# Kernel optimization log

Hardware: AMD Instinct MI355X
Metric: run time of the kernel (lower is better)

The kernel has to match this reference:

```python
import jax, jax.numpy as jnp
import numpy as np

SEQ, WORD, EMBED, NHEAD = 2048, 1024, 128, 16


def setup_inputs() -> dict:
    key = jax.random.key(0)
    ks = jax.random.split(key, 6)
    sw = 1.0 / np.sqrt(WORD)  # xavier-ish scale for linear weights
    sp = 1.0 / np.sqrt(EMBED * NHEAD)
    return {
        "x": jax.random.normal(ks[0], (SEQ, WORD), jnp.float32),
        "Wq": jax.random.normal(ks[1], (NHEAD, WORD, EMBED), jnp.float32) * sw,
        "bq": jnp.zeros((NHEAD, EMBED), jnp.float32),
        "Wk": jax.random.normal(ks[2], (NHEAD, WORD, EMBED), jnp.float32) * sw,
        "bk": jnp.zeros((NHEAD, EMBED), jnp.float32),
        "Wv": jax.random.normal(ks[3], (NHEAD, WORD, EMBED), jnp.float32) * sw,
        "bv": jnp.zeros((NHEAD, EMBED), jnp.float32),
        "proj": jax.random.normal(ks[4], (NHEAD * EMBED, EMBED), jnp.float32) * sp,
    }


def reference(x, Wq, bq, Wk, bk, Wv, bv, proj):
    # Batched-head equivalent of the per-head Attention ModuleList loop.
    # x: [S, W]; Wq/Wk/Wv: [H, W, E]; b*: [H, E]; proj: [H*E, E]
    Q = jnp.einsum("sw,hwe->hse", x, Wq) + bq[:, None, :]
    K = jnp.einsum("sw,hwe->hse", x, Wk) + bk[:, None, :]
    V = jnp.einsum("sw,hwe->hse", x, Wv) + bv[:, None, :]
    scale = 1.0 / jnp.sqrt(jnp.asarray(EMBED, x.dtype))
    scores = jnp.einsum("hqe,hke->hqk", Q, K) * scale  # [H, S, S]
    attn = jax.nn.softmax(scores, axis=-1)
    Z = jnp.einsum("hqk,hke->hqe", attn, V)  # [H, S, E]
    # torch.cat([...], dim=1): per-head outputs side-by-side -> [S, H*E]
    Z_s = jnp.transpose(Z, (1, 0, 2)).reshape(x.shape[0], -1)
    return Z_s @ proj  # [S, E]
```

## Files before the change

kernel.cpp:

```cpp
#include <hip/hip_runtime.h>
#include <stdint.h>

#define GAS __attribute__((address_space(1)))
#define LAS __attribute__((address_space(3)))

typedef unsigned short u16;
typedef __attribute__((ext_vector_type(8))) __bf16 bf16x8;
typedef __attribute__((ext_vector_type(4))) float f32x4;

#define SEQ 2048
#define WORD 1024
#define EMBED 128
#define NHEAD 16

__device__ __forceinline__ u16 f2b(float f) {
  return __builtin_bit_cast(u16, (__bf16)f);
}

__global__ __launch_bounds__(256) void cast_x_kernel(const float* __restrict__ x,
                                                     u16* __restrict__ xb) {
  int i = (blockIdx.x * 256 + threadIdx.x) * 4;
  float4 v = *(const float4*)(x + i);
  ushort4 o;
  o.x = f2b(v.x); o.y = f2b(v.y); o.z = f2b(v.z); o.w = f2b(v.w);
  *(ushort4*)(xb + i) = o;
}

__global__ __launch_bounds__(256) void transpose_cast_kernel(
    const float* __restrict__ s0, const float* __restrict__ s1,
    const float* __restrict__ s2, u16* __restrict__ d0, u16* __restrict__ d1,
    u16* __restrict__ d2, int R, int C, long stride, int zsel) {
  __shared__ float tile[32][33];
  const float* s;
  u16* d;
  if (zsel) {
    int z = blockIdx.z;
    int wsel = z >> 4, hh = z & 15;
    s = (wsel == 0 ? s0 : wsel == 1 ? s1 : s2) + (long)hh * stride;
    d = (wsel == 0 ? d0 : wsel == 1 ? d1 : d2) + (long)hh * stride;
  } else {
    s = s0; d = d0;
  }
  int r0 = blockIdx.x * 32, c0 = blockIdx.y * 32;
  int tx = threadIdx.x & 31, ty = threadIdx.x >> 5;
#pragma unroll
  for (int i = 0; i < 4; ++i)
    tile[ty + i * 8][tx] = s[(long)(r0 + ty + i * 8) * C + c0 + tx];
  __syncthreads();
#pragma unroll
  for (int i = 0; i < 4; ++i)
    d[(long)(c0 + ty + i * 8) * R + r0 + tx] = f2b(tile[tx][ty + i * 8]);
}

template <typename OUT>
__device__ __forceinline__ void gemm128(const u16* __restrict__ A, const u16* __restrict__ B,
                                        OUT* __restrict__ C, int lda, int ldb, int ldc,
                                        int ksteps, const float* biasN, const float* biasM,
                                        float scale) {
  __shared__ u16 lA[128 * 64];
  __shared__ u16 lB[128 * 64];
  const int tid = threadIdx.x;
  const int l = tid & 63, w = tid >> 6;
  const int quad = l >> 4, ln = l & 15;
  const int wm = w >> 1, wn = w & 1;
  f32x4 acc[4][4] = {};
  for (int ks = 0; ks < ksteps; ++ks) {
    const u16* Ak = A + ks * 64;
    const u16* Bk = B + ks * 64;
    __syncthreads();
#pragma unroll
    for (int i = 0; i < 4; ++i) {
      int idx = w * 256 + i * 64 + l;
      int r = idx >> 3, cp = idx & 7;
      int cg = cp ^ (r & 7);
      __builtin_amdgcn_global_load_lds((const GAS void*)(Ak + (long)r * lda + cg * 8),
                                       (LAS void*)(lA + (w * 256 + i * 64) * 8), 16, 0, 0);
      __builtin_amdgcn_global_load_lds((const GAS void*)(Bk + (long)r * ldb + cg * 8),
                                       (LAS void*)(lB + (w * 256 + i * 64) * 8), 16, 0, 0);
    }
    __syncthreads();
    bf16x8 af[2][4], bfv[2][4];
#pragma unroll
    for (int kc = 0; kc < 2; ++kc) {
#pragma unroll
      for (int i = 0; i < 4; ++i) {
        int c = kc * 4 + quad;
        int rm = wm * 64 + i * 16 + ln;
        af[kc][i] = *(const bf16x8*)(lA + rm * 64 + ((c ^ (rm & 7)) * 8));
        int rn = wn * 64 + i * 16 + ln;
        bfv[kc][i] = *(const bf16x8*)(lB + rn * 64 + ((c ^ (rn & 7)) * 8));
      }
    }
#pragma unroll
    for (int kc = 0; kc < 2; ++kc)
#pragma unroll
      for (int i = 0; i < 4; ++i)
#pragma unroll
        for (int j = 0; j < 4; ++j)
          acc[i][j] = __builtin_amdgcn_mfma_f32_16x16x32_bf16(af[kc][i], bfv[kc][j],
                                                              acc[i][j], 0, 0, 0);
  }
#pragma unroll
  for (int i = 0; i < 4; ++i) {
#pragma unroll
    for (int j = 0; j < 4; ++j) {
      int row0 = wm * 64 + i * 16 + quad * 4;
      int col = wn * 64 + j * 16 + ln;
      float bn = biasN ? biasN[col] : 0.f;
#pragma unroll
      for (int reg = 0; reg < 4; ++reg) {
        int row = row0 + reg;
        float bm = biasM ? biasM[row] : 0.f;
        float v = (acc[i][j][reg] + bn + bm) * scale;
        if constexpr (sizeof(OUT) == 2)
          C[(long)row * ldc + col] = (OUT)f2b(v);
        else
          C[(long)row * ldc + col] = v;
      }
    }
  }
}

__global__ __launch_bounds__(256, 3) void qkv_gemm_kernel(
    const u16* __restrict__ xb, const u16* __restrict__ Wqt, const u16* __restrict__ Wkt,
    const u16* __restrict__ Wvt, const float* __restrict__ bq, const float* __restrict__ bk,
    const float* __restrict__ bv, u16* __restrict__ Q, u16* __restrict__ Kb,
    u16* __restrict__ Vt) {
  const int t = blockIdx.x;
  const int h = blockIdx.y;
  const int which = blockIdx.z;
  const float qscale = 0.12753042123789493f;
  if (which == 0) {
    gemm128<u16>(xb + t * 128 * WORD, Wqt + h * EMBED * WORD,
                 Q + h * SEQ * EMBED + t * 128 * EMBED, WORD, WORD, EMBED,
                 WORD / 64, bq + h * EMBED, nullptr, qscale);
  } else if (which == 1) {
    gemm128<u16>(xb + t * 128 * WORD, Wkt + h * EMBED * WORD,
                 Kb + h * SEQ * EMBED + t * 128 * EMBED, WORD, WORD, EMBED,
                 WORD / 64, bk + h * EMBED, nullptr, 1.f);
  } else {
    gemm128<u16>(Wvt + h * EMBED * WORD, xb + t * 128 * WORD,
                 Vt + h * EMBED * SEQ + t * 128, WORD, WORD, SEQ,
                 WORD / 64, nullptr, bv + h * EMBED, 1.f);
  }
}

__global__ __launch_bounds__(256, 1) void attn_kernel(const u16* __restrict__ Q,
                                                      const u16* __restrict__ K,
                                                      const u16* __restrict__ V,
                                                      u16* __restrict__ Zs) {
  __shared__ u16 lKV[2][2][16384];
  __shared__ u16 lP[4 * 16 * 72];
  const int h = blockIdx.y, qb = blockIdx.x;
  const int tid = threadIdx.x;
  const int l = tid & 63, w = tid >> 6, quad = l >> 4, ln = l & 15;
  const int wr = w >> 1, wk = w & 1;
  const u16* Qh = Q + h * SEQ * EMBED;
  const u16* Kh = K + h * SEQ * EMBED;
  const u16* Vh = V + h * EMBED * SEQ;
  u16* Pw = lP + w * (16 * 72);
  const int q0 = qb * 128 + wr * 64;

  bf16x8 qf[4][4];
#pragma unroll
  for (int rs = 0; rs < 4; ++rs)
#pragma unroll
    for (int kc = 0; kc < 4; ++kc)
      qf[rs][kc] = *(const bf16x8*)(Qh + (q0 + rs * 16 + ln) * EMBED + kc * 32 + quad * 8);

  const __bf16 ov = (ln == 0) ? (__bf16)1.0f : (__bf16)0.0f;
  const bf16x8 onesf = {ov, ov, ov, ov, ov, ov, ov, ov};

  f32x4 oacc[4][8] = {};
  f32x4 lacc[4] = {};

  auto stage = [&](int sup, int buf) {
#pragma unroll
    for (int j = 0; j < 8; ++j) {
      int cb = j * 256 + w * 64;
      int c = cb + l;
      int r = c >> 4, sc = c & 15, cg = sc ^ (r & 15);
      __builtin_amdgcn_global_load_lds(
          (const GAS void*)(Kh + (sup * 128 + r) * EMBED + cg * 8),
          (LAS void*)(&lKV[buf][0][cb * 8]), 16, 0, 0);
      __builtin_amdgcn_global_load_lds(
          (const GAS void*)(Vh + r * SEQ + sup * 128 + cg * 8),
          (LAS void*)(&lKV[buf][1][cb * 8]), 16, 0, 0);
    }
  };

  stage(0, 0);
  for (int sup = 0; sup < SEQ / 128; ++sup) {
    const int cur = sup & 1;
    __syncthreads();
    if (sup + 1 < SEQ / 128) stage(sup + 1, cur ^ 1);
    const u16* Kb = lKV[cur][0];
    const u16* Vb = lKV[cur][1];
    f32x4 sacc[4][4] = {};
#pragma unroll
    for (int kc = 0; kc < 4; ++kc) {
      bf16x8 kf[4];
#pragma unroll
      for (int ns = 0; ns < 4; ++ns) {
        int kr = wk * 64 + ns * 16 + ln;
        kf[ns] = *(const bf16x8*)(Kb + kr * 128 + (((kc * 4 + quad) ^ (kr & 15)) * 8));
      }
#pragma unroll
      for (int ns = 0; ns < 4; ++ns)
#pragma unroll
        for (int rs = 0; rs < 4; ++rs)
          sacc[rs][ns] = __builtin_amdgcn_mfma_f32_16x16x32_bf16(qf[rs][kc], kf[ns],
                                                                 sacc[rs][ns], 0, 0, 0);
    }
    bf16x8 vf[2][8];
#pragma unroll
    for (int kc2 = 0; kc2 < 2; ++kc2)
#pragma unroll
      for (int es = 0; es < 8; ++es) {
        int er = es * 16 + ln;
        vf[kc2][es] = *(const bf16x8*)(
            Vb + er * 128 + (((wk * 8 + kc2 * 4 + quad) ^ (er & 15)) * 8));
      }
#pragma unroll
    for (int rs = 0; rs < 4; ++rs) {
#pragma unroll
      for (int ns = 0; ns < 4; ++ns)
#pragma unroll
        for (int r = 0; r < 4; ++r)
          Pw[(quad * 4 + r) * 72 + ns * 16 + ln] = f2b(exp2f(sacc[rs][ns][r]));
#pragma unroll
      for (int kc2 = 0; kc2 < 2; ++kc2) {
        bf16x8 pa = *(const bf16x8*)(Pw + ln * 72 + kc2 * 32 + quad * 8);
#pragma unroll
        for (int es = 0; es < 8; ++es)
          oacc[rs][es] = __builtin_amdgcn_mfma_f32_16x16x32_bf16(pa, vf[kc2][es],
                                                                 oacc[rs][es], 0, 0, 0);
        lacc[rs] = __builtin_amdgcn_mfma_f32_16x16x32_bf16(pa, onesf, lacc[rs], 0, 0, 0);
      }
    }
  }
  __syncthreads();
  float* lO = (float*)lKV;
  if (wk == 1) {
#pragma unroll
    for (int rs = 0; rs < 4; ++rs) {
#pragma unroll
      for (int es = 0; es < 8; ++es)
#pragma unroll
        for (int r = 0; r < 4; ++r)
          lO[(wr * 64 + rs * 16 + quad * 4 + r) * 132 + es * 16 + ln] = oacc[rs][es][r];
      if (ln == 0)
#pragma unroll
        for (int r = 0; r < 4; ++r)
          lO[(wr * 64 + rs * 16 + quad * 4 + r) * 132 + 128] = lacc[rs][r];
    }
  }
  __syncthreads();
  if (wk == 0) {
#pragma unroll
    for (int rs = 0; rs < 4; ++rs)
#pragma unroll
      for (int r = 0; r < 4; ++r) {
        int grow = wr * 64 + rs * 16 + quad * 4 + r;
        float lsum = __shfl(lacc[rs][r], l & 48) + lO[grow * 132 + 128];
        float rl = 1.f / lsum;
        int srow = qb * 128 + grow;
#pragma unroll
        for (int es = 0; es < 8; ++es) {
          float o = oacc[rs][es][r] + lO[grow * 132 + es * 16 + ln];
          Zs[(long)srow * (NHEAD * EMBED) + h * EMBED + es * 16 + ln] = f2b(o * rl);
        }
      }
  }
}

__global__ __launch_bounds__(256, 2) void final_gemm_kernel(const u16* __restrict__ Zs,
                                                            const u16* __restrict__ projT,
                                                            float* __restrict__ pbuf) {
  const int t = blockIdx.x;
  const int kc = blockIdx.y;
  gemm128<float>(Zs + (long)t * 128 * (NHEAD * EMBED) + kc * 256, projT + kc * 256,
                 pbuf + (long)kc * SEQ * EMBED + t * 128 * EMBED,
                 NHEAD * EMBED, NHEAD * EMBED, EMBED, 4, nullptr, nullptr, 1.f);
}

__global__ __launch_bounds__(256) void reduce_kernel(const float* __restrict__ pbuf,
                                                     float* __restrict__ out) {
  int i = (blockIdx.x * 256 + threadIdx.x) * 4;
  float4 s = {0.f, 0.f, 0.f, 0.f};
#pragma unroll
  for (int kc = 0; kc < 8; ++kc) {
    float4 v = *(const float4*)(pbuf + (long)kc * SEQ * EMBED + i);
    s.x += v.x; s.y += v.y; s.z += v.z; s.w += v.w;
  }
  *(float4*)(out + i) = s;
}

extern "C" void kernel_launch(void* const* d_in, const int* in_sizes, int n_in,
                              void* d_out, int out_size, void* d_ws, size_t ws_size,
                              hipStream_t stream) {
  const float* x    = (const float*)d_in[0];
  const float* Wq   = (const float*)d_in[1];
  const float* bq   = (const float*)d_in[2];
  const float* Wk   = (const float*)d_in[3];
  const float* bk   = (const float*)d_in[4];
  const float* Wv   = (const float*)d_in[5];
  const float* bv   = (const float*)d_in[6];
  const float* proj = (const float*)d_in[7];
  float* out = (float*)d_out;

  char* ws = (char*)d_ws;
  u16* xb    = (u16*)(ws);
  u16* Wqt   = (u16*)(ws + (4L << 20));
  u16* Wkt   = (u16*)(ws + (8L << 20));
  u16* Wvt   = (u16*)(ws + (12L << 20));
  u16* projT = (u16*)(ws + (16L << 20));
  u16* Qm    = (u16*)(ws + (17L << 20));
  u16* Km    = (u16*)(ws + (26L << 20));
  u16* Vt    = (u16*)(ws + (35L << 20));
  u16* Zs    = (u16*)(ws + (44L << 20));
  float* pbuf = (float*)(ws);

  cast_x_kernel<<<dim3(SEQ * WORD / 1024), dim3(256), 0, stream>>>(x, xb);
  transpose_cast_kernel<<<dim3(WORD / 32, EMBED / 32, 48), dim3(256), 0, stream>>>(
      Wq, Wk, Wv, Wqt, Wkt, Wvt, WORD, EMBED, (long)WORD * EMBED, 1);
  transpose_cast_kernel<<<dim3(SEQ / 32, EMBED / 32, 1), dim3(256), 0, stream>>>(
      proj, nullptr, nullptr, projT, nullptr, nullptr, SEQ, EMBED, 0, 0);

  qkv_gemm_kernel<<<dim3(16, NHEAD, 3), dim3(256), 0, stream>>>(
      xb, Wqt, Wkt, Wvt, bq, bk, bv, Qm, Km, Vt);

  attn_kernel<<<dim3(16, NHEAD), dim3(256), 0, stream>>>(Qm, Km, Vt, Zs);

  final_gemm_kernel<<<dim3(16, 8), dim3(256), 0, stream>>>(Zs, projT, pbuf);
  reduce_kernel<<<dim3(SEQ * EMBED / 1024), dim3(256), 0, stream>>>(pbuf, out);
}
```

Measured before the change: 212.3 us.

## Store Q and V in MFMA fragment layout and split attention keys across waves

The QKV GEMM now writes Q and V directly in MFMA fragment order, so the attention kernel loads them straight from global memory into registers. Only K is staged through LDS. Each attention block now covers 64 queries with all four waves splitting the keys, computing S^T so the P tile packs into a swizzled LDS buffer. The change launches twice as many blocks with two blocks per CU and merges partial outputs through a serial three-step LDS reduction. V fragments now come from global memory on every key step, which adds global traffic and latency risk in exchange for less LDS use and higher occupancy.

Result: slower. 275.3 us (+29.6%).

```diff
diff --git a/kernel.cpp b/kernel.cpp
--- a/kernel.cpp
+++ b/kernel.cpp
@@ -7,6 +7,8 @@
 typedef unsigned short u16;
 typedef __attribute__((ext_vector_type(8))) __bf16 bf16x8;
 typedef __attribute__((ext_vector_type(4))) float f32x4;
+typedef __attribute__((ext_vector_type(4))) unsigned short u16x4;
+typedef __attribute__((ext_vector_type(8))) unsigned short u16x8;
 
 #define SEQ 2048
 #define WORD 1024
@@ -15,6 +17,15 @@
 
 __device__ __forceinline__ u16 f2b(float f) {
   return __builtin_bit_cast(u16, (__bf16)f);
+}
+
+__device__ __forceinline__ long qfrag_off(int qrow, int e) {
+  return ((((long)(qrow >> 4)) * 4 + (e >> 5)) * 64 + ((e >> 3) & 3) * 16 +
+          (qrow & 15)) * 8 + (e & 7);
+}
+__device__ __forceinline__ long vfrag_off(int er, int key) {
+  return (((((long)(key >> 7)) * 4 + ((key >> 5) & 3)) * 8 + (er >> 4)) * 64 +
+          ((key >> 3) & 3) * 16 + (er & 15)) * 8 + (key & 7);
 }
 
 __global__ __launch_bounds__(256) void cast_x_kernel(const float* __restrict__ x,
@@ -52,11 +63,11 @@
     d[(long)(c0 + ty + i * 8) * R + r0 + tx] = f2b(tile[tx][ty + i * 8]);
 }
 
-template <typename OUT>
+template <int MODE>
 __device__ __forceinline__ void gemm128(const u16* __restrict__ A, const u16* __restrict__ B,
-                                        OUT* __restrict__ C, int lda, int ldb, int ldc,
+                                        void* __restrict__ Cp, int lda, int ldb, int ldc,
                                         int ksteps, const float* biasN, const float* biasM,
-                                        float scale) {
+                                        float scale, int rowbase, int colbase) {
   __shared__ u16 lA[128 * 64];
   __shared__ u16 lB[128 * 64];
   const int tid = threadIdx.x;
@@ -112,10 +123,15 @@
         int row = row0 + reg;
         float bm = biasM ? biasM[row] : 0.f;
         float v = (acc[i][j][reg] + bn + bm) * scale;
-        if constexpr (sizeof(OUT) == 2)
-          C[(long)row * ldc + col] = (OUT)f2b(v);
-        else
-          C[(long)row * ldc + col] = v;
+        if constexpr (MODE == 0) {
+          ((float*)Cp)[(long)row * ldc + col] = v;
+        } else if constexpr (MODE == 1) {
+          ((u16*)Cp)[(long)row * ldc + col] = f2b(v);
+        } else if constexpr (MODE == 2) {
+          ((u16*)Cp)[qfrag_off(rowbase + row, colbase + col)] = f2b(v);
+        } else {
+          ((u16*)Cp)[vfrag_off(rowbase + row, colbase + col)] = f2b(v);
+        }
       }
     }
   }
@@ -124,49 +140,47 @@
 __global__ __launch_bounds__(256, 3) void qkv_gemm_kernel(
     const u16* __restrict__ xb, const u16* __restrict__ Wqt, const u16* __restrict__ Wkt,
     const u16* __restrict__ Wvt, const float* __restrict__ bq, const float* __restrict__ bk,
-    const float* __restrict__ bv, u16* __restrict__ Q, u16* __restrict__ Kb,
-    u16* __restrict__ Vt) {
+    const float* __restrict__ bv, u16* __restrict__ Qf, u16* __restrict__ Km,
+    u16* __restrict__ Vf) {
   const int t = blockIdx.x;
   const int h = blockIdx.y;
   const int which = blockIdx.z;
   const float qscale = 0.12753042123789493f;
   if (which == 0) {
-    gemm128<u16>(xb + t * 128 * WORD, Wqt + h * EMBED * WORD,
-                 Q + h * SEQ * EMBED + t * 128 * EMBED, WORD, WORD, EMBED,
-                 WORD / 64, bq + h * EMBED, nullptr, qscale);
+    gemm128<2>(xb + t * 128 * WORD, Wqt + h * EMBED * WORD,
+               Qf + (long)h * 262144, WORD, WORD, 0,
+               WORD / 64, bq + h * EMBED, nullptr, qscale, t * 128, 0);
   } else if (which == 1) {
-    gemm128<u16>(xb + t * 128 * WORD, Wkt + h * EMBED * WORD,
-                 Kb + h * SEQ * EMBED + t * 128 * EMBED, WORD, WORD, EMBED,
-                 WORD / 64, bk + h * EMBED, nullptr, 1.f);
+    gemm128<1>(xb + t * 128 * WORD, Wkt + h * EMBED * WORD,
+               Km + (long)h * SEQ * EMBED + t * 128 * EMBED, WORD, WORD, EMBED,
+               WORD / 64, bk + h * EMBED, nullptr, 1.f, 0, 0);
   } else {
-    gemm128<u16>(Wvt + h * EMBED * WORD, xb + t * 128 * WORD,
-                 Vt + h * EMBED * SEQ + t * 128, WORD, WORD, SEQ,
-                 WORD / 64, nullptr, bv + h * EMBED, 1.f);
-  }
-}
-
-__global__ __launch_bounds__(256, 1) void attn_kernel(const u16* __restrict__ Q,
-                                                      const u16* __restrict__ K,
-                                                      const u16* __restrict__ V,
+    gemm128<3>(Wvt + h * EMBED * WORD, xb + t * 128 * WORD,
+               Vf + (long)h * 262144, WORD, WORD, 0,
+               WORD / 64, nullptr, bv + h * EMBED, 1.f, 0, t * 128);
+  }
+}
+
+__global__ __launch_bounds__(256, 2) void attn_kernel(const u16* __restrict__ Qf,
+                                                      const u16* __restrict__ Km,
+                                                      const u16* __restrict__ Vf,
                                                       u16* __restrict__ Zs) {
-  __shared__ u16 lKV[2][2][16384];
-  __shared__ u16 lP[4 * 16 * 72];
+  __shared__ u16 lK[2][16384];
+  __shared__ u16 lP[4][64 * 32];
   const int h = blockIdx.y, qb = blockIdx.x;
   const int tid = threadIdx.x;
-  const int l = tid & 63, w = tid >> 6, quad = l >> 4, ln = l & 15;
-  const int wr = w >> 1, wk = w & 1;
-  const u16* Qh = Q + h * SEQ * EMBED;
-  const u16* Kh = K + h * SEQ * EMBED;
-  const u16* Vh = V + h * EMBED * SEQ;
-  u16* Pw = lP + w * (16 * 72);
-  const int q0 = qb * 128 + wr * 64;
+  const int l = tid & 63, wk = tid >> 6, quad = l >> 4, ln = l & 15;
+  const u16* Kh = Km + (long)h * SEQ * EMBED;
+  const u16* Qfh = Qf + (long)h * 262144;
+  const u16* Vfh = Vf + (long)h * 262144;
+  u16* Pw = lP[wk];
 
   bf16x8 qf[4][4];
 #pragma unroll
   for (int rs = 0; rs < 4; ++rs)
 #pragma unroll
     for (int kc = 0; kc < 4; ++kc)
-      qf[rs][kc] = *(const bf16x8*)(Qh + (q0 + rs * 16 + ln) * EMBED + kc * 32 + quad * 8);
+      qf[rs][kc] = *(const bf16x8*)(Qfh + (((qb * 4 + rs) * 4 + kc) * 64 + l) * 8);
 
   const __bf16 ov = (ln == 0) ? (__bf16)1.0f : (__bf16)0.0f;
   const bf16x8 onesf = {ov, ov, ov, ov, ov, ov, ov, ov};
@@ -177,15 +191,12 @@
   auto stage = [&](int sup, int buf) {
 #pragma unroll
     for (int j = 0; j < 8; ++j) {
-      int cb = j * 256 + w * 64;
+      int cb = (j * 4 + wk) * 64;
       int c = cb + l;
-      int r = c >> 4, sc = c & 15, cg = sc ^ (r & 15);
+      int kr = c >> 4, cg = (c & 15) ^ (kr & 15);
       __builtin_amdgcn_global_load_lds(
-          (const GAS void*)(Kh + (sup * 128 + r) * EMBED + cg * 8),
-          (LAS void*)(&lKV[buf][0][cb * 8]), 16, 0, 0);
-      __builtin_amdgcn_global_load_lds(
-          (const GAS void*)(Vh + r * SEQ + sup * 128 + cg * 8),
-          (LAS void*)(&lKV[buf][1][cb * 8]), 16, 0, 0);
+          (const GAS void*)(Kh + (sup * 128 + kr) * EMBED + cg * 8),
+          (LAS void*)(&lK[buf][cb * 8]), 16, 0, 0);
     }
   };
 
@@ -193,81 +204,100 @@
   for (int sup = 0; sup < SEQ / 128; ++sup) {
     const int cur = sup & 1;
     __syncthreads();
+    bf16x8 vf0[4];
+#pragma unroll
+    for (int es = 0; es < 4; ++es)
+      vf0[es] = *(const bf16x8*)(Vfh + (((sup * 4 + wk) * 8 + es) * 64 + l) * 8);
     if (sup + 1 < SEQ / 128) stage(sup + 1, cur ^ 1);
-    const u16* Kb = lKV[cur][0];
-    const u16* Vb = lKV[cur][1];
-    f32x4 sacc[4][4] = {};
-#pragma unroll
-    for (int kc = 0; kc < 4; ++kc) {
-      bf16x8 kf[4];
-#pragma unroll
-      for (int ns = 0; ns < 4; ++ns) {
-        int kr = wk * 64 + ns * 16 + ln;
-        kf[ns] = *(const bf16x8*)(Kb + kr * 128 + (((kc * 4 + quad) ^ (kr & 15)) * 8));
-      }
-#pragma unroll
-      for (int ns = 0; ns < 4; ++ns)
+    const u16* Kb = lK[cur];
+#pragma unroll
+    for (int ns = 0; ns < 2; ++ns) {
+      f32x4 sacc[4] = {};
+#pragma unroll
+      for (int kc = 0; kc < 4; ++kc) {
+        int kr = wk * 32 + ns * 16 + ln;
+        bf16x8 kf = *(const bf16x8*)(Kb + kr * 128 + (((kc * 4 + quad) ^ ln) * 8));
 #pragma unroll
         for (int rs = 0; rs < 4; ++rs)
-          sacc[rs][ns] = __builtin_amdgcn_mfma_f32_16x16x32_bf16(qf[rs][kc], kf[ns],
-                                                                 sacc[rs][ns], 0, 0, 0);
-    }
-    bf16x8 vf[2][8];
-#pragma unroll
-    for (int kc2 = 0; kc2 < 2; ++kc2)
-#pragma unroll
-      for (int es = 0; es < 8; ++es) {
-        int er = es * 16 + ln;
-        vf[kc2][es] = *(const bf16x8*)(
-            Vb + er * 128 + (((wk * 8 + kc2 * 4 + quad) ^ (er & 15)) * 8));
-      }
+          sacc[rs] = __builtin_amdgcn_mfma_f32_16x16x32_bf16(kf, qf[rs][kc],
+                                                             sacc[rs], 0, 0, 0);
+      }
+#pragma unroll
+      for (int rs = 0; rs < 4; ++rs) {
+        u16x4 pk;
+        pk.x = f2b(exp2f(sacc[rs][0]));
+        pk.y = f2b(exp2f(sacc[rs][1]));
+        pk.z = f2b(exp2f(sacc[rs][2]));
+        pk.w = f2b(exp2f(sacc[rs][3]));
+        *(u16x4*)(Pw + (rs * 16 + ln) * 32 + ((ns * 4 + quad) ^ (ln & 7)) * 4) = pk;
+      }
+    }
+    bf16x8 pa[4];
 #pragma unroll
     for (int rs = 0; rs < 4; ++rs) {
-#pragma unroll
-      for (int ns = 0; ns < 4; ++ns)
-#pragma unroll
-        for (int r = 0; r < 4; ++r)
-          Pw[(quad * 4 + r) * 72 + ns * 16 + ln] = f2b(exp2f(sacc[rs][ns][r]));
-#pragma unroll
-      for (int kc2 = 0; kc2 < 2; ++kc2) {
-        bf16x8 pa = *(const bf16x8*)(Pw + ln * 72 + kc2 * 32 + quad * 8);
+      u16x4 lo = *(const u16x4*)(Pw + (rs * 16 + ln) * 32 + ((2 * quad) ^ (ln & 7)) * 4);
+      u16x4 hi = *(const u16x4*)(Pw + (rs * 16 + ln) * 32 + ((2 * quad + 1) ^ (ln & 7)) * 4);
+      u16x8 cc = {lo.x, lo.y, lo.z, lo.w, hi.x, hi.y, hi.z, hi.w};
+      pa[rs] = __builtin_bit_cast(bf16x8, cc);
+    }
+    bf16x8 vf1[4];
+#pragma unroll
+    for (int es = 0; es < 4; ++es)
+      vf1[es] = *(const bf16x8*)(Vfh + (((sup * 4 + wk) * 8 + es + 4) * 64 + l) * 8);
+#pragma unroll
+    for (int es = 0; es < 4; ++es)
+#pragma unroll
+      for (int rs = 0; rs < 4; ++rs)
+        oacc[rs][es] = __builtin_amdgcn_mfma_f32_16x16x32_bf16(pa[rs], vf0[es],
+                                                               oacc[rs][es], 0, 0, 0);
+#pragma unroll
+    for (int es = 0; es < 4; ++es)
+#pragma unroll
+      for (int rs = 0; rs < 4; ++rs)
+        oacc[rs][es + 4] = __builtin_amdgcn_mfma_f32_16x16x32_bf16(pa[rs], vf1[es],
+                                                                   oacc[rs][es + 4], 0, 0, 0);
+#pragma unroll
+    for (int rs = 0; rs < 4; ++rs)
+      lacc[rs] = __builtin_amdgcn_mfma_f32_16x16x32_bf16(pa[rs], onesf, lacc[rs], 0, 0, 0);
+  }
+  __syncthreads();
+  float* lO = (float*)&lK[0][0];
+  float* lL = (float*)&lK[1][0];
+  for (int st = 3; st >= 1; --st) {
+    if (wk == st) {
+#pragma unroll
+      for (int rs = 0; rs < 4; ++rs) {
 #pragma unroll
         for (int es = 0; es < 8; ++es)
-          oacc[rs][es] = __builtin_amdgcn_mfma_f32_16x16x32_bf16(pa, vf[kc2][es],
-                                                                 oacc[rs][es], 0, 0, 0);
-        lacc[rs] = __builtin_amdgcn_mfma_f32_16x16x32_bf16(pa, onesf, lacc[rs], 0, 0, 0);
-      }
-    }
-  }
-  __syncthreads();
-  float* lO = (float*)lKV;
-  if (wk == 1) {
-#pragma unroll
-    for (int rs = 0; rs < 4; ++rs) {
-#pragma unroll
-      for (int es = 0; es < 8; ++es)
-#pragma unroll
-        for (int r = 0; r < 4; ++r)
-          lO[(wr * 64 + rs * 16 + quad * 4 + r) * 132 + es * 16 + ln] = oacc[rs][es][r];
-      if (ln == 0)
-#pragma unroll
-        for (int r = 0; r < 4; ++r)
-          lO[(wr * 64 + rs * 16 + quad * 4 + r) * 132 + 128] = lacc[rs][r];
-    }
-  }
-  __syncthreads();
+#pragma unroll
+          for (int r = 0; r < 4; ++r) {
+            int idx = (rs * 16 + quad * 4 + r) * 128 + es * 16 + ln;
+            if (st == 3) lO[idx] = oacc[rs][es][r];
+            else lO[idx] += oacc[rs][es][r];
+          }
+        if (ln == 0)
+#pragma unroll
+          for (int r = 0; r < 4; ++r) {
+            int row = rs * 16 + quad * 4 + r;
+            if (st == 3) lL[row] = lacc[rs][r];
+            else lL[row] += lacc[rs][r];
+          }
+      }
+    }
+    __syncthreads();
+  }
   if (wk == 0) {
 #pragma unroll
     for (int rs = 0; rs < 4; ++rs)
 #pragma unroll
       for (int r = 0; r < 4; ++r) {
-        int grow = wr * 64 + rs * 16 + quad * 4 + r;
-        float lsum = __shfl(lacc[rs][r], l & 48) + lO[grow * 132 + 128];
+        int row = rs * 16 + quad * 4 + r;
+        float lsum = __shfl(lacc[rs][r], l & 48) + lL[row];
         float rl = 1.f / lsum;
-        int srow = qb * 128 + grow;
+        int srow = qb * 64 + row;
 #pragma unroll
         for (int es = 0; es < 8; ++es) {
-          float o = oacc[rs][es][r] + lO[grow * 132 + es * 16 + ln];
+          float o = oacc[rs][es][r] + lO[row * 128 + es * 16 + ln];
           Zs[(long)srow * (NHEAD * EMBED) + h * EMBED + es * 16 + ln] = f2b(o * rl);
         }
       }
@@ -279,9 +309,9 @@
                                                             float* __restrict__ pbuf) {
   const int t = blockIdx.x;
   const int kc = blockIdx.y;
-  gemm128<float>(Zs + (long)t * 128 * (NHEAD * EMBED) + kc * 256, projT + kc * 256,
-                 pbuf + (long)kc * SEQ * EMBED + t * 128 * EMBED,
-                 NHEAD * EMBED, NHEAD * EMBED, EMBED, 4, nullptr, nullptr, 1.f);
+  gemm128<0>(Zs + (long)t * 128 * (NHEAD * EMBED) + kc * 256, projT + kc * 256,
+             pbuf + (long)kc * SEQ * EMBED + t * 128 * EMBED,
+             NHEAD * EMBED, NHEAD * EMBED, EMBED, 4, nullptr, nullptr, 1.f, 0, 0);
 }
 
 __global__ __launch_bounds__(256) void reduce_kernel(const float* __restrict__ pbuf,
@@ -315,9 +345,9 @@
   u16* Wkt   = (u16*)(ws + (8L << 20));
   u16* Wvt   = (u16*)(ws + (12L << 20));
   u16* projT = (u16*)(ws + (16L << 20));
-  u16* Qm    = (u16*)(ws + (17L << 20));
+  u16* Qf    = (u16*)(ws + (17L << 20));
   u16* Km    = (u16*)(ws + (26L << 20));
-  u16* Vt    = (u16*)(ws + (35L << 20));
+  u16* Vf    = (u16*)(ws + (35L << 20));
   u16* Zs    = (u16*)(ws + (44L << 20));
   float* pbuf = (float*)(ws);
 
@@ -328,9 +358,9 @@
       proj, nullptr, nullptr, projT, nullptr, nullptr, SEQ, EMBED, 0, 0);
 
   qkv_gemm_kernel<<<dim3(16, NHEAD, 3), dim3(256), 0, stream>>>(
-      xb, Wqt, Wkt, Wvt, bq, bk, bv, Qm, Km, Vt);
-
-  attn_kernel<<<dim3(16, NHEAD), dim3(256), 0, stream>>>(Qm, Km, Vt, Zs);
+      xb, Wqt, Wkt, Wvt, bq, bk, bv, Qf, Km, Vf);
+
+  attn_kernel<<<dim3(32, NHEAD), dim3(256), 0, stream>>>(Qf, Km, Vf, Zs);
 
   final_gemm_kernel<<<dim3(16, 8), dim3(256), 0, stream>>>(Zs, projT, pbuf);
   reduce_kernel<<<dim3(SEQ * EMBED / 1024), dim3(256), 0, stream>>>(pbuf, out);
```
